# Performance work log

Hardware: AMD Instinct MI355X
Metric: run time of the kernel (lower is better)

## Reference

```python
import jax, jax.numpy as jnp
import numpy as np

K_TOP = 2
N_HEADS = 4

def _ln(x, g, b, eps=1e-5):
    mu = x.mean(-1, keepdims=True)
    var = ((x - mu) ** 2).mean(-1, keepdims=True)
    return (x - mu) * jax.lax.rsqrt(var + eps) * g + b

def setup_inputs() -> dict:
    key = jax.random.key(0)
    ks = jax.random.split(key, 12)
    B, Na, dz, da = 1024, 32, 96, 32
    D = dz + da
    E, F, Hh, nr = 8, 1024, 512, 4
    s = 0.02
    rn = lambda k, sh: jax.random.normal(k, sh, jnp.float32) * s
    return dict(
        z=jax.random.normal(ks[0], (B, Na, dz), jnp.float32),
        a=jax.random.normal(ks[1], (B, Na, da), jnp.float32),
        w_gate=rn(ks[2], (Na * D, E)),
        w_in=rn(ks[3], (E, 3 * D, D)), b_in=jnp.zeros((E, 3 * D), jnp.float32),
        w_out=rn(ks[4], (E, D, D)), b_out=jnp.zeros((E, D), jnp.float32),
        ln1_g=jnp.ones((E, D), jnp.float32), ln1_b=jnp.zeros((E, D), jnp.float32),
        w1=rn(ks[5], (E, F, D)), b1=jnp.zeros((E, F), jnp.float32),
        w2=rn(ks[6], (E, D, F)), b2=jnp.zeros((E, D), jnp.float32),
        ln2_g=jnp.ones((E, D), jnp.float32), ln2_b=jnp.zeros((E, D), jnp.float32),
        head_w1=rn(ks[7], (Hh, Na * D)), head_b1=jnp.zeros((Hh,), jnp.float32),
        head_w2=rn(ks[8], (nr, Hh)), head_b2=jnp.zeros((nr,), jnp.float32),
    )

def reference(z, a, w_gate, w_in, b_in, w_out, b_out, ln1_g, ln1_b, w1, b1, w2, b2, ln2_g, ln2_b, head_w1, head_b1, head_w2, head_b2):
    B, Na, _ = z.shape
    x = jnp.concatenate([z, a], axis=-1)          # [B, Na, D]
    D = x.shape[-1]
    E = w_gate.shape[1]
    hd = D // N_HEADS
    x_flat = x.reshape(B, -1)                     # [B, Na*D]

    # --- NoisyTopKRouter (eval: clean logits only) ---
    logits = x_flat @ w_gate                      # [B, E]
    top_vals, top_idx = jax.lax.top_k(logits, min(K_TOP + 1, E))
    tk_gates = jax.nn.softmax(top_vals[:, :K_TOP], axis=1)
    gates = jnp.zeros_like(logits).at[jnp.arange(B)[:, None], top_idx[:, :K_TOP]].set(tk_gates)
    load = (gates > 0).sum(0).astype(jnp.float32)
    importance = gates.sum(0)
    cv2 = lambda v: jnp.var(v, ddof=1) / (jnp.mean(v) ** 2 + 1e-10)
    loss_bal = cv2(importance) + cv2(load) + jax.scipy.special.logsumexp(logits, axis=-1).mean()

    # --- expert (self-attn + FFN, pre/post-LN residual) ---
    def expert(p):
        wi, bi, wo, bo, g1, be1, W1, B1, W2, B2, g2, be2 = p
        qkv = x @ wi.T + bi                       # [B, Na, 3D]
        q, k_, v = jnp.split(qkv, 3, axis=-1)
        q = q.reshape(B, Na, N_HEADS, hd)
        k_ = k_.reshape(B, Na, N_HEADS, hd)
        v = v.reshape(B, Na, N_HEADS, hd)
        sc = jnp.einsum('bqhd,bkhd->bhqk', q, k_) / jnp.sqrt(jnp.float32(hd))
        att = jax.nn.softmax(sc, axis=-1)
        o = jnp.einsum('bhqk,bkhd->bqhd', att, v).reshape(B, Na, D)
        o = o @ wo.T + bo
        h = _ln(x + o, g1, be1)
        f = jax.nn.relu(h @ W1.T + B1) @ W2.T + B2
        return _ln(h + f, g2, be2)

    def body(y, p):
        *ep, gate_e = p                           # gate_e: [B]
        y = y + gate_e[:, None, None] * expert(tuple(ep))
        return y, None

    xs = (w_in, b_in, w_out, b_out, ln1_g, ln1_b, w1, b1, w2, b2, ln2_g, ln2_b, gates.T)
    y, _ = jax.lax.scan(body, jnp.zeros_like(x), xs)

    y_flat = y.reshape(B, -1)
    r = jax.nn.relu(y_flat @ head_w1.T + head_b1) @ head_w2.T + head_b2  # [B, n_r]
    return r, gates, loss_bal
```

## Files before the change

### kernel.cpp

```cpp
#include <hip/hip_runtime.h>
#include <math.h>


typedef short bf16x8 __attribute__((ext_vector_type(8)));
typedef float f32x4 __attribute__((ext_vector_type(4)));
typedef unsigned short u16;

#define MFMA(a, b, c) __builtin_amdgcn_mfma_f32_16x16x32_bf16((a), (b), (c), 0, 0, 0)

__device__ __forceinline__ u16 f2bf(float f) {
    unsigned int u = __float_as_uint(f);
    unsigned int r = u + 0x7FFFu + ((u >> 16) & 1u);
    return (u16)(r >> 16);
}
__device__ __forceinline__ float bf2f(u16 s) {
    return __uint_as_float(((unsigned int)s) << 16);
}

__global__ __launch_bounds__(256) void convert_kernel(
    const float* __restrict__ wi, const float* __restrict__ wo,
    const float* __restrict__ w1, const float* __restrict__ w2,
    const float* __restrict__ hw1,
    u16* __restrict__ wiB, u16* __restrict__ woB, u16* __restrict__ w1B,
    u16* __restrict__ w2B, u16* __restrict__ hw1B)
{
    int i4 = blockIdx.x * 256 + threadIdx.x;
    int e = i4 * 4;
    const float* s; u16* d; int off;
    if (e < 393216)       { s = wi;  d = wiB;  off = e; }
    else if (e < 524288)  { s = wo;  d = woB;  off = e - 393216; }
    else if (e < 1572864) { s = w1;  d = w1B;  off = e - 524288; }
    else if (e < 2621440) { s = w2;  d = w2B;  off = e - 1572864; }
    else                  { s = hw1; d = hw1B; off = e - 2621440; }
    float4 v = *(const float4*)(s + off);
    ushort4 o;
    o.x = f2bf(v.x); o.y = f2bf(v.y); o.z = f2bf(v.z); o.w = f2bf(v.w);
    *(ushort4*)(d + off) = o;
}

__global__ __launch_bounds__(256) void router_kernel(
    const float* __restrict__ z, const float* __restrict__ a,
    const float* __restrict__ wg,
    float* __restrict__ gates_out, float* __restrict__ lse_ws,
    int* __restrict__ topi, float* __restrict__ topg)
{
    __shared__ float red[256][9];
    const int b = blockIdx.x, t = threadIdx.x;
    float acc[8];
#pragma unroll
    for (int e = 0; e < 8; ++e) acc[e] = 0.f;
#pragma unroll
    for (int i = 0; i < 16; ++i) {
        int f = i * 256 + t;
        int n = f >> 7, d = f & 127;
        float xv = (d < 96) ? z[(b * 32 + n) * 96 + d]
                            : a[(b * 32 + n) * 32 + d - 96];
        const float* wr = wg + f * 8;
#pragma unroll
        for (int e = 0; e < 8; ++e) acc[e] += xv * wr[e];
    }
#pragma unroll
    for (int e = 0; e < 8; ++e) red[t][e] = acc[e];
    __syncthreads();
    for (int s = 128; s; s >>= 1) {
        if (t < s) {
#pragma unroll
            for (int e = 0; e < 8; ++e) red[t][e] += red[t + s][e];
        }
        __syncthreads();
    }
    if (t == 0) {
        float L[8];
#pragma unroll
        for (int e = 0; e < 8; ++e) L[e] = red[0][e];
        int i0 = 0;
#pragma unroll
        for (int e = 1; e < 8; ++e) if (L[e] > L[i0]) i0 = e;
        int i1 = -1; float v1 = -3.0e38f;
#pragma unroll
        for (int e = 0; e < 8; ++e) if (e != i0 && L[e] > v1) { v1 = L[e]; i1 = e; }
        float e1 = expf(v1 - L[i0]);
        float inv = 1.f / (1.f + e1);
        float g0 = inv, g1 = e1 * inv;
#pragma unroll
        for (int e = 0; e < 8; ++e)
            gates_out[b * 8 + e] = (e == i0) ? g0 : ((e == i1) ? g1 : 0.f);
        float m = L[i0];
        float se = 0.f;
#pragma unroll
        for (int e = 0; e < 8; ++e) se += expf(L[e] - m);
        lse_ws[b] = m + logf(se);
        topi[b * 2 + 0] = i0; topi[b * 2 + 1] = i1;
        topg[b * 2 + 0] = g0; topg[b * 2 + 1] = g1;
    }
}

__global__ __launch_bounds__(1024) void build_loss_kernel(
    const int* __restrict__ topi, const float* __restrict__ topg,
    const float* __restrict__ lse,
    int* __restrict__ cnts, int* __restrict__ ent, int* __restrict__ meta,
    float* __restrict__ out_loss)
{
    __shared__ int sc_[8];
    __shared__ int toff[8];
    __shared__ float red[9][1024];
    const int t = threadIdx.x;
    if (t < 8) sc_[t] = 0;
    __syncthreads();
    int e0 = topi[t * 2], e1 = topi[t * 2 + 1];
    float g0 = topg[t * 2], g1 = topg[t * 2 + 1];
    int p0 = atomicAdd(&sc_[e0], 1);
    ent[e0 * 1024 + p0] = t * 2;
    int p1 = atomicAdd(&sc_[e1], 1);
    ent[e1 * 1024 + p1] = t * 2 + 1;
#pragma unroll
    for (int e = 0; e < 8; ++e)
        red[e][t] = ((e == e0) ? g0 : 0.f) + ((e == e1) ? g1 : 0.f);
    red[8][t] = lse[t];
    __syncthreads();
    for (int s = 512; s; s >>= 1) {
        if (t < s) {
#pragma unroll
            for (int q = 0; q < 9; ++q) red[q][t] += red[q][t + s];
        }
        __syncthreads();
    }
    if (t == 0) {
        int off = 0;
        for (int e = 0; e < 8; ++e) { toff[e] = off; off += (sc_[e] + 1) >> 1; }
        meta[0] = off;
        float cvv[2];
        for (int p = 0; p < 2; ++p) {
            float v[8], sum = 0.f;
            for (int e = 0; e < 8; ++e) {
                v[e] = p ? (float)sc_[e] : red[e][0];
                sum += v[e];
            }
            float mean = sum * (1.f / 8.f);
            float var = 0.f;
            for (int e = 0; e < 8; ++e) { float d = v[e] - mean; var += d * d; }
            var *= (1.f / 7.f);
            cvv[p] = var / (mean * mean + 1e-10f);
        }
        out_loss[0] = cvv[0] + cvv[1] + red[8][0] * (1.f / 1024.f);
    }
    __syncthreads();
    if (t < 8) {
        cnts[t] = sc_[t];
        int ntl = (sc_[t] + 1) >> 1, o = toff[t];
        for (int j = 0; j < ntl; ++j) {
            meta[1 + 2 * (o + j)] = t;
            meta[2 + 2 * (o + j)] = j * 2;
        }
    }
}

#define SM_X 0
#define SM_Q 16384
#define SM_K 32768
#define SM_V 49152
#define SM_TOT 65536
#define PS_OFF 0
#define PQ_OFF 1024
#define MU_OFF 2048
#define RS_OFF 2304
#define NTILES 1028

__device__ __forceinline__ int tsw(int row, int col) {
    return row * 256 + ((col * 2) ^ ((row & 7) << 4));
}
__device__ __forceinline__ int vsw(int row, int col) {
    return row * 128 + ((col * 2) ^ ((row & 7) << 4));
}

__global__ __launch_bounds__(512, 2) void expert_group_kernel(
    const float* __restrict__ z, const float* __restrict__ a,
    const u16* __restrict__ wiBF, const float* __restrict__ b_in,
    const u16* __restrict__ woBF, const float* __restrict__ b_out,
    const float* __restrict__ ln1g, const float* __restrict__ ln1b,
    const u16* __restrict__ w1BF, const float* __restrict__ b1,
    const u16* __restrict__ w2BF, const float* __restrict__ b2,
    const float* __restrict__ ln2g, const float* __restrict__ ln2b,
    const float* __restrict__ topg, const int* __restrict__ cnts,
    const int* __restrict__ meta, const int* __restrict__ ent,
    u16* __restrict__ ybf)
{
    __shared__ __align__(16) char sm[SM_TOT];
    const int n_tiles = meta[0];
    const int bid = blockIdx.x;
    if (bid >= n_tiles) return;
    const int e = meta[1 + 2 * bid], base = meta[2 + 2 * bid];
    const int cnt = cnts[e];

    const int t = threadIdx.x;
    const int w = t >> 6, l = t & 63, l16 = l & 15, lk = l >> 4;
    const int ke = lk * 8;
    const int wr = w >> 2, wc = w & 3;
    const f32x4 zv = {0.f, 0.f, 0.f, 0.f};

    int bs[2], valid[2]; float gg[2];
#pragma unroll
    for (int i = 0; i < 2; ++i) {
        int gi = base + i;
        int idx = (gi < cnt) ? gi : (cnt - 1);
        int code = ent[e * 1024 + idx];
        valid[i] = (gi < cnt);
        bs[i] = code;
        gg[i] = topg[code];
    }

#pragma unroll
    for (int i = 0; i < 2; ++i) {
        int cid = i * 512 + t;
        int row = cid >> 4;
        int cb = (cid & 15) * 8;
        int b_ = bs[row >> 5] >> 1;
        int n = row & 31;
        float4 p0, p1;
        if (cb < 96) {
            const float* zp = z + ((size_t)b_ * 32 + n) * 96 + cb;
            p0 = *(const float4*)zp; p1 = *(const float4*)(zp + 4);
        } else {
            const float* ap = a + ((size_t)b_ * 32 + n) * 32 + (cb - 96);
            p0 = *(const float4*)ap; p1 = *(const float4*)(ap + 4);
        }
        bf16x8 pk;
        pk[0] = (short)f2bf(p0.x); pk[1] = (short)f2bf(p0.y);
        pk[2] = (short)f2bf(p0.z); pk[3] = (short)f2bf(p0.w);
        pk[4] = (short)f2bf(p1.x); pk[5] = (short)f2bf(p1.y);
        pk[6] = (short)f2bf(p1.z); pk[7] = (short)f2bf(p1.w);
        *(bf16x8*)(sm + SM_X + tsw(row, cb)) = pk;
    }
    __syncthreads();

    {
        f32x4 acc[2][6];
#pragma unroll
        for (int mt = 0; mt < 2; ++mt)
#pragma unroll
            for (int q = 0; q < 6; ++q) acc[mt][q] = zv;
#pragma unroll
        for (int ks = 0; ks < 4; ++ks) {
            bf16x8 af[2];
#pragma unroll
            for (int mt = 0; mt < 2; ++mt) {
                int R = wr * 32 + mt * 16 + l16;
                af[mt] = *(const bf16x8*)(sm + SM_X + tsw(R, ks * 32 + ke));
            }
#pragma unroll
            for (int q = 0; q < 6; ++q) {
                int j = wc * 96 + q * 16 + l16;
                bf16x8 bb = *(const bf16x8*)(wiBF + e * 49152 + j * 128 + ks * 32 + ke);
#pragma unroll
                for (int mt = 0; mt < 2; ++mt) acc[mt][q] = MFMA(af[mt], bb, acc[mt][q]);
            }
        }
#pragma unroll
        for (int q = 0; q < 6; ++q) {
            int C = wc * 96 + q * 16 + l16;
            float bj = b_in[e * 384 + C];
#pragma unroll
            for (int mt = 0; mt < 2; ++mt)
#pragma unroll
                for (int i = 0; i < 4; ++i) {
                    int R = wr * 32 + mt * 16 + lk * 4 + i;
                    u16 val = f2bf(acc[mt][q][i] + bj);
                    if (C < 128) {
                        *(u16*)(sm + SM_Q + tsw(R, C)) = val;
                    } else if (C < 256) {
                        *(u16*)(sm + SM_K + tsw(R, C - 128)) = val;
                    } else {
                        *(u16*)(sm + SM_V + vsw(C - 256, R)) = val;
                    }
                }
        }
    }
    __syncthreads();

    {
        const int tok = w >> 2, hb = (w & 3) * 32;
        const float scale = 0.17677669529663687f;
        bf16x8 qa[2], kf[2];
#pragma unroll
        for (int mt = 0; mt < 2; ++mt) {
            int R = tok * 32 + mt * 16 + l16;
            qa[mt] = *(const bf16x8*)(sm + SM_Q + tsw(R, hb + ke));
            kf[mt] = *(const bf16x8*)(sm + SM_K + tsw(R, hb + ke));
        }
        f32x4 sc[2][2];
        sc[0][0] = MFMA(qa[0], kf[0], zv); sc[0][1] = MFMA(qa[0], kf[1], zv);
        sc[1][0] = MFMA(qa[1], kf[0], zv); sc[1][1] = MFMA(qa[1], kf[1], zv);
#pragma unroll
        for (int mt = 0; mt < 2; ++mt)
#pragma unroll
            for (int i = 0; i < 4; ++i) {
                float v0 = sc[mt][0][i] * scale, v1 = sc[mt][1][i] * scale;
                float m = fmaxf(v0, v1);
                m = fmaxf(m, __shfl_xor(m, 1)); m = fmaxf(m, __shfl_xor(m, 2));
                m = fmaxf(m, __shfl_xor(m, 4)); m = fmaxf(m, __shfl_xor(m, 8));
                float e0 = __expf(v0 - m), e1 = __expf(v1 - m);
                float ssum = e0 + e1;
                ssum += __shfl_xor(ssum, 1); ssum += __shfl_xor(ssum, 2);
                ssum += __shfl_xor(ssum, 4); ssum += __shfl_xor(ssum, 8);
                float inv = 1.f / ssum;
                int row = mt * 16 + lk * 4 + i;
                char* pb = sm + SM_X + w * 2048 + row * 64;
                int sw = (row & 3) << 4;
                *(u16*)(pb + ((l16 * 2) ^ sw)) = f2bf(e0 * inv);
                *(u16*)(pb + (((16 + l16) * 2) ^ sw)) = f2bf(e1 * inv);
            }
        bf16x8 pa[2];
#pragma unroll
        for (int mt = 0; mt < 2; ++mt) {
            int row = mt * 16 + l16;
            pa[mt] = *(const bf16x8*)(sm + SM_X + w * 2048 + row * 64 +
                                      ((ke * 2) ^ ((row & 3) << 4)));
        }
        f32x4 o[2][2];
#pragma unroll
        for (int nt = 0; nt < 2; ++nt) {
            int rv = hb + nt * 16 + l16;
            bf16x8 vb = *(const bf16x8*)(sm + SM_V + vsw(rv, tok * 32 + ke));
            o[0][nt] = MFMA(pa[0], vb, zv);
            o[1][nt] = MFMA(pa[1], vb, zv);
        }
#pragma unroll
        for (int mt = 0; mt < 2; ++mt)
#pragma unroll
            for (int nt = 0; nt < 2; ++nt)
#pragma unroll
                for (int i = 0; i < 4; ++i) {
                    int R = tok * 32 + mt * 16 + lk * 4 + i;
                    int C = hb + nt * 16 + l16;
                    *(u16*)(sm + SM_Q + tsw(R, C)) = f2bf(o[mt][nt][i]);
                }
    }
    __syncthreads();

    {
        f32x4 pr[2][2];
        pr[0][0] = zv; pr[0][1] = zv; pr[1][0] = zv; pr[1][1] = zv;
#pragma unroll
        for (int ks = 0; ks < 4; ++ks) {
            bf16x8 af[2];
#pragma unroll
            for (int mt = 0; mt < 2; ++mt) {
                int R = wr * 32 + mt * 16 + l16;
                af[mt] = *(const bf16x8*)(sm + SM_Q + tsw(R, ks * 32 + ke));
            }
#pragma unroll
            for (int nt = 0; nt < 2; ++nt) {
                int j = wc * 32 + nt * 16 + l16;
                bf16x8 bb = *(const bf16x8*)(woBF + e * 16384 + j * 128 + ks * 32 + ke);
                pr[0][nt] = MFMA(af[0], bb, pr[0][nt]);
                pr[1][nt] = MFMA(af[1], bb, pr[1][nt]);
            }
        }
        int C0 = wc * 32 + l16, C1 = C0 + 16;
        float bo0 = b_out[e * 128 + C0];
        float bo1 = b_out[e * 128 + C1];
        int b_ = bs[wr] >> 1;
#pragma unroll
        for (int mt = 0; mt < 2; ++mt)
#pragma unroll
            for (int i = 0; i < 4; ++i) {
                int R = wr * 32 + mt * 16 + lk * 4 + i;
                int n = R & 31;
                float x0 = (C0 < 96) ? z[((size_t)b_ * 32 + n) * 96 + C0]
                                     : a[((size_t)b_ * 32 + n) * 32 + C0 - 96];
                float x1 = (C1 < 96) ? z[((size_t)b_ * 32 + n) * 96 + C1]
                                     : a[((size_t)b_ * 32 + n) * 32 + C1 - 96];
                float u0 = pr[mt][0][i] + bo0 + x0;
                float u1v = pr[mt][1][i] + bo1 + x1;
                *(u16*)(sm + SM_K + tsw(R, C0)) = f2bf(u0);
                *(u16*)(sm + SM_K + tsw(R, C1)) = f2bf(u1v);
                float s = u0 + u1v;
                float q = u0 * u0 + u1v * u1v;
                s += __shfl_xor(s, 1); q += __shfl_xor(q, 1);
                s += __shfl_xor(s, 2); q += __shfl_xor(q, 2);
                s += __shfl_xor(s, 4); q += __shfl_xor(q, 4);
                s += __shfl_xor(s, 8); q += __shfl_xor(q, 8);
                if (l16 == 0) {
                    *(float*)(sm + SM_X + PS_OFF + (R * 4 + wc) * 4) = s;
                    *(float*)(sm + SM_X + PQ_OFF + (R * 4 + wc) * 4) = q;
                }
            }
    }
    __syncthreads();
    if (t < 64) {
        float s = 0.f, q = 0.f;
#pragma unroll
        for (int c = 0; c < 4; ++c) {
            s += *(const float*)(sm + SM_X + PS_OFF + (t * 4 + c) * 4);
            q += *(const float*)(sm + SM_X + PQ_OFF + (t * 4 + c) * 4);
        }
        float mu = s * (1.f / 128.f);
        float var = q * (1.f / 128.f) - mu * mu;
        *(float*)(sm + SM_X + MU_OFF + t * 4) = mu;
        *(float*)(sm + SM_X + RS_OFF + t * 4) = rsqrtf(var + 1e-5f);
    }
    __syncthreads();
    {
        int r_ = t >> 3, c0 = (t & 7) * 16;
        float mu_ = *(const float*)(sm + SM_X + MU_OFF + r_ * 4);
        float rs_ = *(const float*)(sm + SM_X + RS_OFF + r_ * 4);
#pragma unroll
        for (int j4 = 0; j4 < 2; ++j4) {
            int cb = c0 + j4 * 8;
            bf16x8* p = (bf16x8*)(sm + SM_K + tsw(r_, cb));
            bf16x8 vch = *p;
#pragma unroll
            for (int jj = 0; jj < 8; ++jj) {
                int c = cb + jj;
                float f = (bf2f((u16)vch[jj]) - mu_) * rs_ * ln1g[e * 128 + c] + ln1b[e * 128 + c];
                vch[jj] = (short)f2bf(f);
            }
            *p = vch;
        }
    }
    __syncthreads();

    f32x4 facc[2][2];
    facc[0][0] = zv; facc[0][1] = zv; facc[1][0] = zv; facc[1][1] = zv;
    {
        bf16x8 w1f[2][4], w2f[2][4];
#pragma unroll
        for (int nt = 0; nt < 2; ++nt)
#pragma unroll
            for (int ks = 0; ks < 4; ++ks) {
                int j = wc * 32 + nt * 16 + l16;
                w1f[nt][ks] = *(const bf16x8*)(w1BF + e * 131072 + j * 128 + ks * 32 + ke);
            }
        for (int c = 0; c < 8; ++c) {
#pragma unroll
            for (int nt = 0; nt < 2; ++nt)
#pragma unroll
                for (int ks = 0; ks < 4; ++ks) {
                    int j = wc * 32 + nt * 16 + l16;
                    w2f[nt][ks] = *(const bf16x8*)(w2BF + e * 131072 + j * 1024 +
                                                   c * 128 + ks * 32 + ke);
                }
            f32x4 a1[2][2];
            a1[0][0] = zv; a1[0][1] = zv; a1[1][0] = zv; a1[1][1] = zv;
#pragma unroll
            for (int ks = 0; ks < 4; ++ks) {
                bf16x8 af[2];
#pragma unroll
                for (int mt = 0; mt < 2; ++mt) {
                    int R = wr * 32 + mt * 16 + l16;
                    af[mt] = *(const bf16x8*)(sm + SM_K + tsw(R, ks * 32 + ke));
                }
#pragma unroll
                for (int mt = 0; mt < 2; ++mt) {
                    a1[mt][0] = MFMA(af[mt], w1f[0][ks], a1[mt][0]);
                    a1[mt][1] = MFMA(af[mt], w1f[1][ks], a1[mt][1]);
                }
            }
            char* Fb = sm + ((c & 1) ? SM_V : SM_Q);
            float b10 = b1[e * 1024 + c * 128 + wc * 32 + l16];
            float b11 = b1[e * 1024 + c * 128 + wc * 32 + 16 + l16];
#pragma unroll
            for (int mt = 0; mt < 2; ++mt)
#pragma unroll
                for (int nt = 0; nt < 2; ++nt)
#pragma unroll
                    for (int i = 0; i < 4; ++i) {
                        int R = wr * 32 + mt * 16 + lk * 4 + i;
                        int C = wc * 32 + nt * 16 + l16;
                        *(u16*)(Fb + tsw(R, C)) =
                            f2bf(fmaxf(a1[mt][nt][i] + (nt ? b11 : b10), 0.f));
                    }
            if (c < 7) {
#pragma unroll
                for (int nt = 0; nt < 2; ++nt)
#pragma unroll
                    for (int ks = 0; ks < 4; ++ks) {
                        int j = (c + 1) * 128 + wc * 32 + nt * 16 + l16;
                        w1f[nt][ks] = *(const bf16x8*)(w1BF + e * 131072 + j * 128 + ks * 32 + ke);
                    }
            }
            __syncthreads();
#pragma unroll
            for (int ks = 0; ks < 4; ++ks) {
                bf16x8 af[2];
#pragma unroll
                for (int mt = 0; mt < 2; ++mt) {
                    int R = wr * 32 + mt * 16 + l16;
                    af[mt] = *(const bf16x8*)(Fb + tsw(R, ks * 32 + ke));
                }
#pragma unroll
                for (int mt = 0; mt < 2; ++mt) {
                    facc[mt][0] = MFMA(af[mt], w2f[0][ks], facc[mt][0]);
                    facc[mt][1] = MFMA(af[mt], w2f[1][ks], facc[mt][1]);
                }
            }
        }
    }

    {
        int C0 = wc * 32 + l16, C1 = C0 + 16;
        float b20 = b2[e * 128 + C0];
        float b21 = b2[e * 128 + C1];
        float u2[2][2][4];
#pragma unroll
        for (int mt = 0; mt < 2; ++mt)
#pragma unroll
            for (int i = 0; i < 4; ++i) {
                int R = wr * 32 + mt * 16 + lk * 4 + i;
                float h0 = bf2f(*(const u16*)(sm + SM_K + tsw(R, C0)));
                float h1v = bf2f(*(const u16*)(sm + SM_K + tsw(R, C1)));
                u2[mt][0][i] = facc[mt][0][i] + b20 + h0;
                u2[mt][1][i] = facc[mt][1][i] + b21 + h1v;
                float s = u2[mt][0][i] + u2[mt][1][i];
                float q = u2[mt][0][i] * u2[mt][0][i] + u2[mt][1][i] * u2[mt][1][i];
                s += __shfl_xor(s, 1); q += __shfl_xor(q, 1);
                s += __shfl_xor(s, 2); q += __shfl_xor(q, 2);
                s += __shfl_xor(s, 4); q += __shfl_xor(q, 4);
                s += __shfl_xor(s, 8); q += __shfl_xor(q, 8);
                if (l16 == 0) {
                    *(float*)(sm + SM_X + PS_OFF + (R * 4 + wc) * 4) = s;
                    *(float*)(sm + SM_X + PQ_OFF + (R * 4 + wc) * 4) = q;
                }
            }
        __syncthreads();
        if (t < 64) {
            float s = 0.f, q = 0.f;
#pragma unroll
            for (int c = 0; c < 4; ++c) {
                s += *(const float*)(sm + SM_X + PS_OFF + (t * 4 + c) * 4);
                q += *(const float*)(sm + SM_X + PQ_OFF + (t * 4 + c) * 4);
            }
            float mu = s * (1.f / 128.f);
            float var = q * (1.f / 128.f) - mu * mu;
            *(float*)(sm + SM_X + MU_OFF + t * 4) = mu;
            *(float*)(sm + SM_X + RS_OFF + t * 4) = rsqrtf(var + 1e-5f);
        }
        __syncthreads();
        float g20 = ln2g[e * 128 + C0], g21 = ln2g[e * 128 + C1];
        float e20 = ln2b[e * 128 + C0], e21 = ln2b[e * 128 + C1];
        float gm = gg[wr];
#pragma unroll
        for (int mt = 0; mt < 2; ++mt)
#pragma unroll
            for (int i = 0; i < 4; ++i) {
                int R = wr * 32 + mt * 16 + lk * 4 + i;
                float mu_ = *(const float*)(sm + SM_X + MU_OFF + R * 4);
                float rs_ = *(const float*)(sm + SM_X + RS_OFF + R * 4);
                float v0 = gm * ((u2[mt][0][i] - mu_) * rs_ * g20 + e20);
                float v1 = gm * ((u2[mt][1][i] - mu_) * rs_ * g21 + e21);
                *(u16*)(sm + SM_Q + tsw(R, C0)) = f2bf(v0);
                *(u16*)(sm + SM_Q + tsw(R, C1)) = f2bf(v1);
            }
    }
    __syncthreads();
#pragma unroll
    for (int i = 0; i < 2; ++i) {
        int cid = i * 512 + t;
        int r_ = cid >> 4, cb = (cid & 15) * 8;
        int ei = r_ >> 5;
        if (valid[ei]) {
            int code = bs[ei];
            int b_ = code >> 1, s_ = code & 1;
            u16* dst = ybf + ((size_t)(s_ * 1024 + b_)) * 4096 + (r_ & 31) * 128 + cb;
            *(bf16x8*)dst = *(const bf16x8*)(sm + SM_Q + tsw(r_, cb));
        }
    }
}

__global__ __launch_bounds__(256) void combine_kernel(
    u16* __restrict__ y0, const u16* __restrict__ y1)
{
    int i = (blockIdx.x * 256 + threadIdx.x) * 8;
    bf16x8 a = *(const bf16x8*)(y0 + i);
    bf16x8 b = *(const bf16x8*)(y1 + i);
    bf16x8 o;
#pragma unroll
    for (int j = 0; j < 8; ++j)
        o[j] = (short)f2bf(bf2f((u16)a[j]) + bf2f((u16)b[j]));
    *(bf16x8*)(y0 + i) = o;
}

__global__ __launch_bounds__(256) void head1_mfma(
    const u16* __restrict__ y_bf, const u16* __restrict__ hw1BF,
    const float* __restrict__ hb1, float* __restrict__ h_act)
{
    const int t = threadIdx.x, w = t >> 6, l = t & 63, l16 = l & 15, lk = l >> 4;
    const int ke = lk * 8;
    const int mb = blockIdx.x * 32, cb = blockIdx.y * 64 + w * 16;
    const f32x4 zv = {0.f, 0.f, 0.f, 0.f};
    f32x4 acc[2]; acc[0] = zv; acc[1] = zv;
    const u16* arow0 = y_bf + (size_t)(mb + l16) * 4096;
    const u16* arow1 = y_bf + (size_t)(mb + 16 + l16) * 4096;
    const u16* brow  = hw1BF + (size_t)(cb + l16) * 4096;
    for (int k0 = 0; k0 < 4096; k0 += 32) {
        bf16x8 a0 = *(const bf16x8*)(arow0 + k0 + ke);
        bf16x8 a1 = *(const bf16x8*)(arow1 + k0 + ke);
        bf16x8 bb = *(const bf16x8*)(brow + k0 + ke);
        acc[0] = MFMA(a0, bb, acc[0]);
        acc[1] = MFMA(a1, bb, acc[1]);
    }
    int col = cb + l16;
    float bv = hb1[col];
#pragma unroll
    for (int mt = 0; mt < 2; ++mt)
#pragma unroll
        for (int i = 0; i < 4; ++i) {
            int row = mb + mt * 16 + lk * 4 + i;
            h_act[(size_t)row * 512 + col] = fmaxf(acc[mt][i] + bv, 0.f);
        }
}

__global__ __launch_bounds__(64) void head2_kernel(
    const float* __restrict__ h_act, const float* __restrict__ w2,
    const float* __restrict__ b2, float* __restrict__ r)
{
    const int b = blockIdx.x, t = threadIdx.x;
    float a0 = 0.f, a1 = 0.f, a2 = 0.f, a3 = 0.f;
    for (int h = t; h < 512; h += 64) {
        float hv = h_act[b * 512 + h];
        a0 += hv * w2[h];
        a1 += hv * w2[512 + h];
        a2 += hv * w2[1024 + h];
        a3 += hv * w2[1536 + h];
    }
#pragma unroll
    for (int off = 32; off; off >>= 1) {
        a0 += __shfl_down(a0, off);
        a1 += __shfl_down(a1, off);
        a2 += __shfl_down(a2, off);
        a3 += __shfl_down(a3, off);
    }
    if (t == 0) {
        r[b * 4 + 0] = a0 + b2[0];
        r[b * 4 + 1] = a1 + b2[1];
        r[b * 4 + 2] = a2 + b2[2];
        r[b * 4 + 3] = a3 + b2[3];
    }
}

extern "C" void kernel_launch(void* const* d_in, const int* in_sizes, int n_in,
                              void* d_out, int out_size, void* d_ws, size_t ws_size,
                              hipStream_t stream) {
    const float* z    = (const float*)d_in[0];
    const float* a    = (const float*)d_in[1];
    const float* wg   = (const float*)d_in[2];
    const float* w_in = (const float*)d_in[3];
    const float* b_in = (const float*)d_in[4];
    const float* w_o  = (const float*)d_in[5];
    const float* b_o  = (const float*)d_in[6];
    const float* l1g  = (const float*)d_in[7];
    const float* l1b  = (const float*)d_in[8];
    const float* w1   = (const float*)d_in[9];
    const float* b1   = (const float*)d_in[10];
    const float* w2   = (const float*)d_in[11];
    const float* b2   = (const float*)d_in[12];
    const float* l2g  = (const float*)d_in[13];
    const float* l2b  = (const float*)d_in[14];
    const float* hw1  = (const float*)d_in[15];
    const float* hb1  = (const float*)d_in[16];
    const float* hw2  = (const float*)d_in[17];
    const float* hb2  = (const float*)d_in[18];

    float* out = (float*)d_out;
    float* r_out     = out;
    float* gates_out = out + 4096;
    float* loss_out  = out + 12288;

    char* W = (char*)d_ws;
    u16*   wiBF  = (u16*)(W + 0);
    u16*   woBF  = (u16*)(W + 786432);
    u16*   w1BF  = (u16*)(W + 1048576);
    u16*   w2BF  = (u16*)(W + 3145728);
    u16*   hw1BF = (u16*)(W + 5242880);
    u16*   ybf   = (u16*)(W + 9437184);
    float* h_act = (float*)(W + 26214400);
    float* lse   = (float*)(W + 28311552);
    float* topg  = (float*)(W + 28315648);
    int*   topi  = (int*)  (W + 28323840);
    int*   cnts  = (int*)  (W + 28332032);
    int*   meta  = (int*)  (W + 28332160);
    int*   ent   = (int*)  (W + 28340480);

    convert_kernel<<<4608, 256, 0, stream>>>(w_in, w_o, w1, w2, hw1,
                                             wiBF, woBF, w1BF, w2BF, hw1BF);
    router_kernel<<<1024, 256, 0, stream>>>(z, a, wg, gates_out, lse, topi, topg);
    build_loss_kernel<<<1, 1024, 0, stream>>>(topi, topg, lse, cnts, ent, meta, loss_out);
    expert_group_kernel<<<NTILES, 512, 0, stream>>>(z, a, wiBF, b_in, woBF, b_o,
        l1g, l1b, w1BF, b1, w2BF, b2, l2g, l2b, topg, cnts, meta, ent, ybf);
    combine_kernel<<<2048, 256, 0, stream>>>(ybf, ybf + 4194304);
    head1_mfma<<<dim3(32, 8), 256, 0, stream>>>(ybf, hw1BF, hb1, h_act);
    head2_kernel<<<1024, 64, 0, stream>>>(h_act, hw2, hb2, r_out);
}
```

Measured before the change: 348.6 us.

## Split expert kernel into attention and FFN kernels with larger FFN tiles

Splits the fused expert kernel in two. An attention kernel processes 64 rows per block and writes the post-LN1 activations to a global buffer. A separate FFN kernel then processes 256 rows (8 tokens) per block, so each W1/W2 weight fragment fetched from global memory is reused across four times as many rows. The goal is to cut the repeated weight traffic of the small 64-row FFN tiles, at the cost of an extra global round trip for the intermediate activations, one more launch, and 128KB of LDS per FFN block (the kernel still declares two blocks per CU in its launch bounds).

After: 424.3 us. 21.7% more time.

```diff
diff --git a/kernel.cpp b/kernel.cpp
--- a/kernel.cpp
+++ b/kernel.cpp
@@ -99,10 +99,11 @@
     const int* __restrict__ topi, const float* __restrict__ topg,
     const float* __restrict__ lse,
     int* __restrict__ cnts, int* __restrict__ ent, int* __restrict__ meta,
-    float* __restrict__ out_loss)
+    int* __restrict__ metaF, float* __restrict__ out_loss)
 {
     __shared__ int sc_[8];
     __shared__ int toff[8];
+    __shared__ int toffF[8];
     __shared__ float red[9][1024];
     const int t = threadIdx.x;
     if (t < 8) sc_[t] = 0;
@@ -110,9 +111,9 @@
     int e0 = topi[t * 2], e1 = topi[t * 2 + 1];
     float g0 = topg[t * 2], g1 = topg[t * 2 + 1];
     int p0 = atomicAdd(&sc_[e0], 1);
-    ent[e0 * 1024 + p0] = t * 2;
+    ent[e0 * 2048 + p0] = t * 2;
     int p1 = atomicAdd(&sc_[e1], 1);
-    ent[e1 * 1024 + p1] = t * 2 + 1;
+    ent[e1 * 2048 + p1] = t * 2 + 1;
 #pragma unroll
     for (int e = 0; e < 8; ++e)
         red[e][t] = ((e == e0) ? g0 : 0.f) + ((e == e1) ? g1 : 0.f);
@@ -126,9 +127,13 @@
         __syncthreads();
     }
     if (t == 0) {
-        int off = 0;
-        for (int e = 0; e < 8; ++e) { toff[e] = off; off += (sc_[e] + 1) >> 1; }
+        int off = 0, offF = 0;
+        for (int e = 0; e < 8; ++e) {
+            toff[e] = off;   off  += (sc_[e] + 1) >> 1;
+            toffF[e] = offF; offF += (sc_[e] + 7) >> 3;
+        }
         meta[0] = off;
+        metaF[0] = offF;
         float cvv[2];
         for (int p = 0; p < 2; ++p) {
             float v[8], sum = 0.f;
@@ -151,6 +156,11 @@
         for (int j = 0; j < ntl; ++j) {
             meta[1 + 2 * (o + j)] = t;
             meta[2 + 2 * (o + j)] = j * 2;
+        }
+        int ntlF = (sc_[t] + 7) >> 3, oF = toffF[t];
+        for (int j = 0; j < ntlF; ++j) {
+            metaF[1 + 2 * (oF + j)] = t;
+            metaF[2 + 2 * (oF + j)] = j * 8;
         }
     }
 }
@@ -173,17 +183,14 @@
     return row * 128 + ((col * 2) ^ ((row & 7) << 4));
 }
 
-__global__ __launch_bounds__(512, 2) void expert_group_kernel(
+__global__ __launch_bounds__(512, 2) void attn_kernel(
     const float* __restrict__ z, const float* __restrict__ a,
     const u16* __restrict__ wiBF, const float* __restrict__ b_in,
     const u16* __restrict__ woBF, const float* __restrict__ b_out,
     const float* __restrict__ ln1g, const float* __restrict__ ln1b,
-    const u16* __restrict__ w1BF, const float* __restrict__ b1,
-    const u16* __restrict__ w2BF, const float* __restrict__ b2,
-    const float* __restrict__ ln2g, const float* __restrict__ ln2b,
-    const float* __restrict__ topg, const int* __restrict__ cnts,
-    const int* __restrict__ meta, const int* __restrict__ ent,
-    u16* __restrict__ ybf)
+    const int* __restrict__ cnts, const int* __restrict__ meta,
+    const int* __restrict__ ent,
+    u16* __restrict__ h1g)
 {
     __shared__ __align__(16) char sm[SM_TOT];
     const int n_tiles = meta[0];
@@ -198,15 +205,12 @@
     const int wr = w >> 2, wc = w & 3;
     const f32x4 zv = {0.f, 0.f, 0.f, 0.f};
 
-    int bs[2], valid[2]; float gg[2];
+    int bs[2];
 #pragma unroll
     for (int i = 0; i < 2; ++i) {
         int gi = base + i;
         int idx = (gi < cnt) ? gi : (cnt - 1);
-        int code = ent[e * 1024 + idx];
-        valid[i] = (gi < cnt);
-        bs[i] = code;
-        gg[i] = topg[code];
+        bs[i] = ent[e * 2048 + idx];
     }
 
 #pragma unroll
@@ -419,151 +423,191 @@
         }
     }
     __syncthreads();
-
-    f32x4 facc[2][2];
-    facc[0][0] = zv; facc[0][1] = zv; facc[1][0] = zv; facc[1][1] = zv;
+#pragma unroll
+    for (int i = 0; i < 2; ++i) {
+        int cid = i * 512 + t;
+        int r_ = cid >> 4, cb = (cid & 15) * 8;
+        int code = bs[r_ >> 5];
+        u16* dst = h1g + (size_t)code * 4096 + (r_ & 31) * 128 + cb;
+        *(bf16x8*)dst = *(const bf16x8*)(sm + SM_K + tsw(r_, cb));
+    }
+}
+
+#define FH 0
+#define FF 65536
+#define NF_TILES 264
+
+__global__ __launch_bounds__(512, 2) void ffn_kernel(
+    const u16* __restrict__ h1g,
+    const u16* __restrict__ w1BF, const float* __restrict__ b1,
+    const u16* __restrict__ w2BF, const float* __restrict__ b2,
+    const float* __restrict__ ln2g, const float* __restrict__ ln2b,
+    const float* __restrict__ topg, const int* __restrict__ cnts,
+    const int* __restrict__ metaF, const int* __restrict__ ent,
+    u16* __restrict__ ybf)
+{
+    __shared__ __align__(16) char sm[131072];
+    const int nf = metaF[0];
+    const int bid = blockIdx.x;
+    if (bid >= nf) return;
+    const int e = metaF[1 + 2 * bid], base = metaF[2 + 2 * bid];
+    const int cnt = cnts[e];
+
+    const int t = threadIdx.x;
+    const int w = t >> 6, l = t & 63, l16 = l & 15, lk = l >> 4;
+    const int ke = lk * 8;
+    const int wr = w >> 1, wc = w & 1;
+    const f32x4 zv = {0.f, 0.f, 0.f, 0.f};
+
+    int code8[8]; float gg8[8];
+#pragma unroll
+    for (int i = 0; i < 8; ++i) {
+        int gi = base + i;
+        int idx = (gi < cnt) ? gi : (cnt - 1);
+        code8[i] = ent[e * 2048 + idx];
+        gg8[i] = topg[code8[i]];
+    }
+
+#pragma unroll
+    for (int it = 0; it < 8; ++it) {
+        int cid = it * 512 + t;
+        int row = cid >> 4, cb = (cid & 15) * 8;
+        int code = code8[row >> 5];
+        *(bf16x8*)(sm + FH + tsw(row, cb)) =
+            *(const bf16x8*)(h1g + (size_t)code * 4096 + (row & 31) * 128 + cb);
+    }
+    __syncthreads();
+
+    f32x4 facc[4][4];
+#pragma unroll
+    for (int mt = 0; mt < 4; ++mt)
+#pragma unroll
+        for (int nt = 0; nt < 4; ++nt) facc[mt][nt] = zv;
+
+    for (int c = 0; c < 8; ++c) {
+        f32x4 a1[4][4];
+#pragma unroll
+        for (int mt = 0; mt < 4; ++mt)
+#pragma unroll
+            for (int nt = 0; nt < 4; ++nt) a1[mt][nt] = zv;
+#pragma unroll
+        for (int ks = 0; ks < 4; ++ks) {
+            bf16x8 af[4];
+#pragma unroll
+            for (int mt = 0; mt < 4; ++mt) {
+                int R = wr * 64 + mt * 16 + l16;
+                af[mt] = *(const bf16x8*)(sm + FH + tsw(R, ks * 32 + ke));
+            }
+#pragma unroll
+            for (int nt = 0; nt < 4; ++nt) {
+                int j = c * 128 + wc * 64 + nt * 16 + l16;
+                bf16x8 bb = *(const bf16x8*)(w1BF + e * 131072 + j * 128 + ks * 32 + ke);
+#pragma unroll
+                for (int mt = 0; mt < 4; ++mt) a1[mt][nt] = MFMA(af[mt], bb, a1[mt][nt]);
+            }
+        }
+        __syncthreads();
+#pragma unroll
+        for (int nt = 0; nt < 4; ++nt) {
+            int C = wc * 64 + nt * 16 + l16;
+            float bv = b1[e * 1024 + c * 128 + C];
+#pragma unroll
+            for (int mt = 0; mt < 4; ++mt)
+#pragma unroll
+                for (int i = 0; i < 4; ++i) {
+                    int R = wr * 64 + mt * 16 + lk * 4 + i;
+                    *(u16*)(sm + FF + tsw(R, C)) = f2bf(fmaxf(a1[mt][nt][i] + bv, 0.f));
+                }
+        }
+        __syncthreads();
+#pragma unroll
+        for (int ks = 0; ks < 4; ++ks) {
+            bf16x8 af[4];
+#pragma unroll
+            for (int mt = 0; mt < 4; ++mt) {
+                int R = wr * 64 + mt * 16 + l16;
+                af[mt] = *(const bf16x8*)(sm + FF + tsw(R, ks * 32 + ke));
+            }
+#pragma unroll
+            for (int nt = 0; nt < 4; ++nt) {
+                int j = wc * 64 + nt * 16 + l16;
+                bf16x8 bb = *(const bf16x8*)(w2BF + e * 131072 + j * 1024 +
+                                             c * 128 + ks * 32 + ke);
+#pragma unroll
+                for (int mt = 0; mt < 4; ++mt) facc[mt][nt] = MFMA(af[mt], bb, facc[mt][nt]);
+            }
+        }
+    }
+    __syncthreads();
+
+    float sp[16], qp[16];
     {
-        bf16x8 w1f[2][4], w2f[2][4];
-#pragma unroll
-        for (int nt = 0; nt < 2; ++nt)
-#pragma unroll
-            for (int ks = 0; ks < 4; ++ks) {
-                int j = wc * 32 + nt * 16 + l16;
-                w1f[nt][ks] = *(const bf16x8*)(w1BF + e * 131072 + j * 128 + ks * 32 + ke);
-            }
-        for (int c = 0; c < 8; ++c) {
-#pragma unroll
-            for (int nt = 0; nt < 2; ++nt)
-#pragma unroll
-                for (int ks = 0; ks < 4; ++ks) {
-                    int j = wc * 32 + nt * 16 + l16;
-                    w2f[nt][ks] = *(const bf16x8*)(w2BF + e * 131072 + j * 1024 +
-                                                   c * 128 + ks * 32 + ke);
+        float b2v[4];
+#pragma unroll
+        for (int nt = 0; nt < 4; ++nt) b2v[nt] = b2[e * 128 + wc * 64 + nt * 16 + l16];
+#pragma unroll
+        for (int mt = 0; mt < 4; ++mt)
+#pragma unroll
+            for (int i = 0; i < 4; ++i) {
+                int R = wr * 64 + mt * 16 + lk * 4 + i;
+                float s = 0.f, q = 0.f;
+#pragma unroll
+                for (int nt = 0; nt < 4; ++nt) {
+                    int C = wc * 64 + nt * 16 + l16;
+                    float h = bf2f(*(const u16*)(sm + FH + tsw(R, C)));
+                    float u = facc[mt][nt][i] + b2v[nt] + h;
+                    *(u16*)(sm + FF + tsw(R, C)) = f2bf(u);
+                    s += u; q += u * u;
                 }
-            f32x4 a1[2][2];
-            a1[0][0] = zv; a1[0][1] = zv; a1[1][0] = zv; a1[1][1] = zv;
-#pragma unroll
-            for (int ks = 0; ks < 4; ++ks) {
-                bf16x8 af[2];
-#pragma unroll
-                for (int mt = 0; mt < 2; ++mt) {
-                    int R = wr * 32 + mt * 16 + l16;
-                    af[mt] = *(const bf16x8*)(sm + SM_K + tsw(R, ks * 32 + ke));
-                }
-#pragma unroll
-                for (int mt = 0; mt < 2; ++mt) {
-                    a1[mt][0] = MFMA(af[mt], w1f[0][ks], a1[mt][0]);
-                    a1[mt][1] = MFMA(af[mt], w1f[1][ks], a1[mt][1]);
-                }
-            }
-            char* Fb = sm + ((c & 1) ? SM_V : SM_Q);
-            float b10 = b1[e * 1024 + c * 128 + wc * 32 + l16];
-            float b11 = b1[e * 1024 + c * 128 + wc * 32 + 16 + l16];
-#pragma unroll
-            for (int mt = 0; mt < 2; ++mt)
-#pragma unroll
-                for (int nt = 0; nt < 2; ++nt)
-#pragma unroll
-                    for (int i = 0; i < 4; ++i) {
-                        int R = wr * 32 + mt * 16 + lk * 4 + i;
-                        int C = wc * 32 + nt * 16 + l16;
-                        *(u16*)(Fb + tsw(R, C)) =
-                            f2bf(fmaxf(a1[mt][nt][i] + (nt ? b11 : b10), 0.f));
-                    }
-            if (c < 7) {
-#pragma unroll
-                for (int nt = 0; nt < 2; ++nt)
-#pragma unroll
-                    for (int ks = 0; ks < 4; ++ks) {
-                        int j = (c + 1) * 128 + wc * 32 + nt * 16 + l16;
-                        w1f[nt][ks] = *(const bf16x8*)(w1BF + e * 131072 + j * 128 + ks * 32 + ke);
-                    }
-            }
-            __syncthreads();
-#pragma unroll
-            for (int ks = 0; ks < 4; ++ks) {
-                bf16x8 af[2];
-#pragma unroll
-                for (int mt = 0; mt < 2; ++mt) {
-                    int R = wr * 32 + mt * 16 + l16;
-                    af[mt] = *(const bf16x8*)(Fb + tsw(R, ks * 32 + ke));
-                }
-#pragma unroll
-                for (int mt = 0; mt < 2; ++mt) {
-                    facc[mt][0] = MFMA(af[mt], w2f[0][ks], facc[mt][0]);
-                    facc[mt][1] = MFMA(af[mt], w2f[1][ks], facc[mt][1]);
-                }
-            }
-        }
-    }
-
-    {
-        int C0 = wc * 32 + l16, C1 = C0 + 16;
-        float b20 = b2[e * 128 + C0];
-        float b21 = b2[e * 128 + C1];
-        float u2[2][2][4];
-#pragma unroll
-        for (int mt = 0; mt < 2; ++mt)
-#pragma unroll
-            for (int i = 0; i < 4; ++i) {
-                int R = wr * 32 + mt * 16 + lk * 4 + i;
-                float h0 = bf2f(*(const u16*)(sm + SM_K + tsw(R, C0)));
-                float h1v = bf2f(*(const u16*)(sm + SM_K + tsw(R, C1)));
-                u2[mt][0][i] = facc[mt][0][i] + b20 + h0;
-                u2[mt][1][i] = facc[mt][1][i] + b21 + h1v;
-                float s = u2[mt][0][i] + u2[mt][1][i];
-                float q = u2[mt][0][i] * u2[mt][0][i] + u2[mt][1][i] * u2[mt][1][i];
                 s += __shfl_xor(s, 1); q += __shfl_xor(q, 1);
                 s += __shfl_xor(s, 2); q += __shfl_xor(q, 2);
                 s += __shfl_xor(s, 4); q += __shfl_xor(q, 4);
                 s += __shfl_xor(s, 8); q += __shfl_xor(q, 8);
-                if (l16 == 0) {
-                    *(float*)(sm + SM_X + PS_OFF + (R * 4 + wc) * 4) = s;
-                    *(float*)(sm + SM_X + PQ_OFF + (R * 4 + wc) * 4) = q;
-                }
-            }
-        __syncthreads();
-        if (t < 64) {
-            float s = 0.f, q = 0.f;
-#pragma unroll
-            for (int c = 0; c < 4; ++c) {
-                s += *(const float*)(sm + SM_X + PS_OFF + (t * 4 + c) * 4);
-                q += *(const float*)(sm + SM_X + PQ_OFF + (t * 4 + c) * 4);
-            }
-            float mu = s * (1.f / 128.f);
-            float var = q * (1.f / 128.f) - mu * mu;
-            *(float*)(sm + SM_X + MU_OFF + t * 4) = mu;
-            *(float*)(sm + SM_X + RS_OFF + t * 4) = rsqrtf(var + 1e-5f);
-        }
-        __syncthreads();
-        float g20 = ln2g[e * 128 + C0], g21 = ln2g[e * 128 + C1];
-        float e20 = ln2b[e * 128 + C0], e21 = ln2b[e * 128 + C1];
-        float gm = gg[wr];
-#pragma unroll
-        for (int mt = 0; mt < 2; ++mt)
+                sp[mt * 4 + i] = s; qp[mt * 4 + i] = q;
+            }
+    }
+    __syncthreads();
+    if (l16 == 0) {
+#pragma unroll
+        for (int mt = 0; mt < 4; ++mt)
 #pragma unroll
             for (int i = 0; i < 4; ++i) {
-                int R = wr * 32 + mt * 16 + lk * 4 + i;
-                float mu_ = *(const float*)(sm + SM_X + MU_OFF + R * 4);
-                float rs_ = *(const float*)(sm + SM_X + RS_OFF + R * 4);
-                float v0 = gm * ((u2[mt][0][i] - mu_) * rs_ * g20 + e20);
-                float v1 = gm * ((u2[mt][1][i] - mu_) * rs_ * g21 + e21);
-                *(u16*)(sm + SM_Q + tsw(R, C0)) = f2bf(v0);
-                *(u16*)(sm + SM_Q + tsw(R, C1)) = f2bf(v1);
-            }
-    }
-    __syncthreads();
-#pragma unroll
-    for (int i = 0; i < 2; ++i) {
-        int cid = i * 512 + t;
-        int r_ = cid >> 4, cb = (cid & 15) * 8;
-        int ei = r_ >> 5;
-        if (valid[ei]) {
-            int code = bs[ei];
-            int b_ = code >> 1, s_ = code & 1;
-            u16* dst = ybf + ((size_t)(s_ * 1024 + b_)) * 4096 + (r_ & 31) * 128 + cb;
-            *(bf16x8*)dst = *(const bf16x8*)(sm + SM_Q + tsw(r_, cb));
-        }
+                int R = wr * 64 + mt * 16 + lk * 4 + i;
+                *(float*)(sm + FH + (R * 2 + wc) * 4) = sp[mt * 4 + i];
+                *(float*)(sm + FH + 2048 + (R * 2 + wc) * 4) = qp[mt * 4 + i];
+            }
+    }
+    __syncthreads();
+    if (t < 256) {
+        float s = *(const float*)(sm + FH + (t * 2) * 4)
+                + *(const float*)(sm + FH + (t * 2 + 1) * 4);
+        float q = *(const float*)(sm + FH + 2048 + (t * 2) * 4)
+                + *(const float*)(sm + FH + 2048 + (t * 2 + 1) * 4);
+        float mu = s * (1.f / 128.f);
+        float var = q * (1.f / 128.f) - mu * mu;
+        *(float*)(sm + FH + 4096 + t * 4) = mu;
+        *(float*)(sm + FH + 5120 + t * 4) = rsqrtf(var + 1e-5f);
+    }
+    __syncthreads();
+#pragma unroll
+    for (int it = 0; it < 8; ++it) {
+        int cid = it * 512 + t;
+        int row = cid >> 4, cb = (cid & 15) * 8;
+        float mu = *(const float*)(sm + FH + 4096 + row * 4);
+        float rs = *(const float*)(sm + FH + 5120 + row * 4);
+        int ei = row >> 5;
+        float gm = gg8[ei];
+        int code = code8[ei];
+        int tok = code >> 1, slot = code & 1;
+        bf16x8 v = *(const bf16x8*)(sm + FF + tsw(row, cb));
+        bf16x8 o;
+#pragma unroll
+        for (int jj = 0; jj < 8; ++jj) {
+            int cc = cb + jj;
+            float f = (bf2f((u16)v[jj]) - mu) * rs * ln2g[e * 128 + cc] + ln2b[e * 128 + cc];
+            o[jj] = (short)f2bf(gm * f);
+        }
+        *(bf16x8*)(ybf + (size_t)(slot * 1024 + tok) * 4096 + (row & 31) * 128 + cb) = o;
     }
 }
 
@@ -673,20 +717,25 @@
     u16*   w2BF  = (u16*)(W + 3145728);
     u16*   hw1BF = (u16*)(W + 5242880);
     u16*   ybf   = (u16*)(W + 9437184);
-    float* h_act = (float*)(W + 26214400);
-    float* lse   = (float*)(W + 28311552);
-    float* topg  = (float*)(W + 28315648);
-    int*   topi  = (int*)  (W + 28323840);
-    int*   cnts  = (int*)  (W + 28332032);
-    int*   meta  = (int*)  (W + 28332160);
-    int*   ent   = (int*)  (W + 28340480);
+    u16*   h1g   = (u16*)(W + 26214400);
+    float* h_act = (float*)(W + 42991616);
+    float* lse   = (float*)(W + 45088768);
+    float* topg  = (float*)(W + 45092864);
+    int*   topi  = (int*)  (W + 45101056);
+    int*   cnts  = (int*)  (W + 45109248);
+    int*   meta  = (int*)  (W + 45109376);
+    int*   metaF = (int*)  (W + 45117696);
+    int*   ent   = (int*)  (W + 45121792);
 
     convert_kernel<<<4608, 256, 0, stream>>>(w_in, w_o, w1, w2, hw1,
                                              wiBF, woBF, w1BF, w2BF, hw1BF);
     router_kernel<<<1024, 256, 0, stream>>>(z, a, wg, gates_out, lse, topi, topg);
-    build_loss_kernel<<<1, 1024, 0, stream>>>(topi, topg, lse, cnts, ent, meta, loss_out);
-    expert_group_kernel<<<NTILES, 512, 0, stream>>>(z, a, wiBF, b_in, woBF, b_o,
-        l1g, l1b, w1BF, b1, w2BF, b2, l2g, l2b, topg, cnts, meta, ent, ybf);
+    build_loss_kernel<<<1, 1024, 0, stream>>>(topi, topg, lse, cnts, ent, meta,
+                                              metaF, loss_out);
+    attn_kernel<<<NTILES, 512, 0, stream>>>(z, a, wiBF, b_in, woBF, b_o,
+        l1g, l1b, cnts, meta, ent, h1g);
+    ffn_kernel<<<NF_TILES, 512, 0, stream>>>(h1g, w1BF, b1, w2BF, b2,
+        l2g, l2b, topg, cnts, metaF, ent, ybf);
     combine_kernel<<<2048, 256, 0, stream>>>(ybf, ybf + 4194304);
     head1_mfma<<<dim3(32, 8), 256, 0, stream>>>(ybf, hw1BF, hb1, h_act);
     head2_kernel<<<1024, 64, 0, stream>>>(h_act, hw2, hb2, r_out);
```
